# Optimization experiments

Measured on AMD Instinct MI355X. Metric: run time of the kernel, lower is better.

The kernel has to match this reference:

```python
import jax, jax.numpy as jnp
import numpy as np

B, T, I = 256, 512, 1024
H, O = 1024, 1024


def setup_inputs() -> dict:
    key = jax.random.key(0)
    ks = jax.random.split(key, 8)
    std = 1.0 / np.sqrt(H)
    u = lambda k, shape: jax.random.uniform(k, shape, jnp.float32, -std, std)
    return {
        "x": jax.random.normal(ks[0], (B, T, I), jnp.float32),
        "Wx": u(ks[1], (4 * H, I)),   # x2h weight
        "bx": u(ks[2], (4 * H,)),     # x2h bias
        "Wh": u(ks[3], (4 * H, H)),   # h2h weight
        "bh": u(ks[4], (4 * H,)),     # h2h bias
        "c2c": u(ks[5], (3 * H,)),    # peephole weights (ci, cf, co)
        "Wfc": u(ks[6], (O, H)),      # final fc weight
        "bfc": u(ks[7], (O,)),        # final fc bias
    }


def reference(x, Wx, bx, Wh, bh, c2c, Wfc, bfc):
    Bv, Tv, _ = x.shape
    Hv = Wh.shape[1]
    # Precompute input projections for all timesteps in one GEMM: [B, T, 4H]
    xg = jnp.einsum('bti,gi->btg', x, Wx) + bx + bh
    ci, cf, co = jnp.split(c2c, 3)

    def step(carry, xg_t):
        h, c = carry                      # [B, H] each
        gates = xg_t + h @ Wh.T           # [B, 4H]
        i, f, g, o = jnp.split(gates, 4, axis=-1)
        i = jax.nn.sigmoid(i + ci * c)    # peephole into input gate
        f = jax.nn.sigmoid(f + cf * c)    # peephole into forget gate
        c_new = f * c + i * jnp.tanh(g)
        o = jax.nn.sigmoid(o + co * c_new)  # peephole into output gate
        h_new = o * jnp.tanh(c_new)
        return (h_new, c_new), None

    h0 = jnp.zeros((Bv, Hv), x.dtype)
    c0 = jnp.zeros((Bv, Hv), x.dtype)
    (hT, _), _ = jax.lax.scan(step, (h0, c0), jnp.swapaxes(xg, 0, 1))
    return hT @ Wfc.T + bfc  # [B, O]
```

## Files before the change

kernel.cpp:

```cpp
#include <hip/hip_runtime.h>
#include <hip/hip_bf16.h>

typedef __attribute__((ext_vector_type(8))) short short8;
typedef __attribute__((ext_vector_type(4))) float f32x4;

#define T_STEPS 512
#define BATCH   256
#define HDIM    1024
#define GDIM    4096

__device__ __forceinline__ float sigmoidf_(float x) {
  return 1.0f / (1.0f + __expf(-x));
}
__device__ __forceinline__ float tanh_(float x) {
  return 2.0f / (1.0f + __expf(-2.0f * x)) - 1.0f;
}
__device__ __forceinline__ short f2bf(float f) {
  __hip_bfloat16 h = __float2bfloat16(f);
  short s;
  __builtin_memcpy(&s, &h, sizeof(short));
  return s;
}

__global__ void pack_kernel(const float* __restrict__ Wh,
                            const float* __restrict__ bx, const float* __restrict__ bh,
                            __hip_bfloat16* __restrict__ Whb,
                            float* __restrict__ biasc)
{
  const int stride = gridDim.x * blockDim.x;
  const int tid0 = blockIdx.x * blockDim.x + threadIdx.x;
  for (int i = tid0; i < GDIM * HDIM; i += stride)
    Whb[i] = __float2bfloat16(Wh[i]);
  for (int i = tid0; i < GDIM; i += stride)
    biasc[i] = bx[i] + bh[i];
}

__global__ __launch_bounds__(512, 1)
void xg_gemm(const float* __restrict__ x, const float* __restrict__ Wx,
             __hip_bfloat16* __restrict__ xg, int t0)
{
  __shared__ short8 As[2][1024];
  __shared__ short8 Bs[2][1024];

  const int tid  = threadIdx.x;
  const int wave = tid >> 6;
  const int lane = tid & 63;

  const int cpx = gridDim.x >> 3;
  const int nb  = (blockIdx.x & 7) * cpx + (blockIdx.x >> 3);
  const int nt  = nb & 31;
  const int mt  = nb >> 5;

  const int trel  = mt >> 1;
  const int brow0 = (mt & 1) * 128;

  const int r0 = tid >> 3;
  const int cg = tid & 7;

  const float* asrc0 = x + ((size_t)(brow0 + r0) * T_STEPS + (t0 + trel)) * 1024 + cg * 8;
  const float* asrc1 = x + ((size_t)(brow0 + r0 + 64) * T_STEPS + (t0 + trel)) * 1024 + cg * 8;
  const float* bsrc0 = Wx + (size_t)(nt * 128 + r0) * 1024 + cg * 8;
  const float* bsrc1 = Wx + (size_t)(nt * 128 + r0 + 64) * 1024 + cg * 8;

  const int aslot0 = r0 * 8 + (cg ^ (r0 & 7));
  const int aslot1 = (r0 + 64) * 8 + (cg ^ (r0 & 7));

  f32x4 a0l, a0h, a1l, a1h, b0l, b0h, b1l, b1h;

#define XG_LOAD(KC)                                        \
  do {                                                     \
    a0l = *(const f32x4*)(asrc0 + (KC) * 64);              \
    a0h = *(const f32x4*)(asrc0 + (KC) * 64 + 4);          \
    a1l = *(const f32x4*)(asrc1 + (KC) * 64);              \
    a1h = *(const f32x4*)(asrc1 + (KC) * 64 + 4);          \
    b0l = *(const f32x4*)(bsrc0 + (KC) * 64);              \
    b0h = *(const f32x4*)(bsrc0 + (KC) * 64 + 4);          \
    b1l = *(const f32x4*)(bsrc1 + (KC) * 64);              \
    b1h = *(const f32x4*)(bsrc1 + (KC) * 64 + 4);          \
  } while (0)

#define XG_CVT1(lo, hi, dstarr, slot)                      \
  do {                                                     \
    short8 s_;                                             \
    _Pragma("unroll")                                      \
    for (int e = 0; e < 4; ++e) {                          \
      s_[e]     = f2bf((lo)[e]);                           \
      s_[e + 4] = f2bf((hi)[e]);                           \
    }                                                      \
    dstarr[slot] = s_;                                     \
  } while (0)

#define XG_WRITE(BUF)                                      \
  do {                                                     \
    XG_CVT1(a0l, a0h, As[BUF], aslot0);                    \
    XG_CVT1(a1l, a1h, As[BUF], aslot1);                    \
    XG_CVT1(b0l, b0h, Bs[BUF], aslot0);                    \
    XG_CVT1(b1l, b1h, Bs[BUF], aslot1);                    \
  } while (0)

  const int wr = wave >> 2;
  const int wc = wave & 3;

  f32x4 acc[4][2];
#pragma unroll
  for (int m = 0; m < 4; ++m)
#pragma unroll
    for (int n = 0; n < 2; ++n) acc[m][n] = (f32x4){0.f, 0.f, 0.f, 0.f};

  XG_LOAD(0);
  XG_WRITE(0);
  __syncthreads();

#pragma unroll 1
  for (int kc = 0; kc < 16; ++kc) {
    if (kc < 15) XG_LOAD(kc + 1);
    const int bs = kc & 1;
#pragma unroll
    for (int ks = 0; ks < 2; ++ks) {
      const int cgf = ks * 4 + (lane >> 4);
      short8 af[4], bfr[2];
#pragma unroll
      for (int m = 0; m < 4; ++m) {
        const int row = wr * 64 + m * 16 + (lane & 15);
        af[m] = As[bs][row * 8 + (cgf ^ (row & 7))];
      }
#pragma unroll
      for (int n = 0; n < 2; ++n) {
        const int row = wc * 32 + n * 16 + (lane & 15);
        bfr[n] = Bs[bs][row * 8 + (cgf ^ (row & 7))];
      }
#pragma unroll
      for (int m = 0; m < 4; ++m)
#pragma unroll
        for (int n = 0; n < 2; ++n)
          acc[m][n] = __builtin_amdgcn_mfma_f32_16x16x32_bf16(af[m], bfr[n], acc[m][n], 0, 0, 0);
    }
    if (kc < 15) XG_WRITE((kc + 1) & 1);
    __syncthreads();
  }

  const int dcol = lane & 15;
  const int dr0  = (lane >> 4) * 4;
#pragma unroll
  for (int m = 0; m < 4; ++m) {
#pragma unroll
    for (int n = 0; n < 2; ++n) {
      const int ocol = nt * 128 + wc * 32 + n * 16 + dcol;
#pragma unroll
      for (int rr = 0; rr < 4; ++rr) {
        const int orow = mt * 128 + wr * 64 + m * 16 + dr0 + rr;
        xg[(size_t)orow * GDIM + ocol] = __float2bfloat16(acc[m][n][rr]);
      }
    }
  }
#undef XG_LOAD
#undef XG_CVT1
#undef XG_WRITE
}

__global__ __launch_bounds__(512, 1)
void lstm_step(const __hip_bfloat16* __restrict__ xg_t,
               const __hip_bfloat16* __restrict__ Whb,
               const float* __restrict__ biasc,
               const float* __restrict__ c2c,
               const __hip_bfloat16* __restrict__ h_in,
               __hip_bfloat16* __restrict__ h_out,
               float* __restrict__ c_st)
{
  __shared__ short8 As[2][1024];
  __shared__ short8 Bs[2][1024];

  const int tid  = threadIdx.x;
  const int wave = tid >> 6;
  const int lane = tid & 63;

  const int bid   = blockIdx.x;
  const int xcd   = bid & 7;
  const int idx   = bid >> 3;
  const int ntile = xcd * 8 + (idx & 7);
  const int mtile = idx >> 3;
  const int b0 = mtile * 64;
  const int j0 = ntile * 16;

  const int r0  = tid >> 4;
  const int cg0 = tid & 15;

  const int aslot0 = r0 * 16 + (cg0 ^ (r0 & 7));
  const int aslot1 = (r0 + 32) * 16 + (cg0 ^ (r0 & 7));

  const int Brow0 = ((r0 >> 4)     ) * HDIM + j0 + (r0 & 15);
  const int Brow1 = ((r0 >> 4) + 2 ) * HDIM + j0 + (r0 & 15);
  const __hip_bfloat16* Wp0 = Whb + (size_t)Brow0 * HDIM + cg0 * 8;
  const __hip_bfloat16* Wp1 = Whb + (size_t)Brow1 * HDIM + cg0 * 8;
  const __hip_bfloat16* hp0 = h_in + (size_t)(b0 + r0) * HDIM + cg0 * 8;
  const __hip_bfloat16* hp1 = h_in + (size_t)(b0 + r0 + 32) * HDIM + cg0 * 8;

  short8 hv0, hv1, bv0, bv1;

#define LOADS(KC)                                                   \
  do {                                                              \
    bv0 = *(const short8*)(const void*)(Wp0 + (size_t)(KC) * 128);  \
    bv1 = *(const short8*)(const void*)(Wp1 + (size_t)(KC) * 128);  \
    hv0 = *(const short8*)(const void*)(hp0 + (size_t)(KC) * 128);  \
    hv1 = *(const short8*)(const void*)(hp1 + (size_t)(KC) * 128);  \
  } while (0)

#define WRITE_LDS(BUF)                                              \
  do {                                                              \
    As[BUF][aslot0] = hv0;                                          \
    As[BUF][aslot1] = hv1;                                          \
    Bs[BUF][aslot0] = bv0;                                          \
    Bs[BUF][aslot1] = bv1;                                          \
  } while (0)

  const int rf = wave & 3;
  const int kh = wave >> 2;
  const int arow = rf * 16 + (lane & 15);

  f32x4 acc[4];
#pragma unroll
  for (int f = 0; f < 4; ++f) acc[f] = (f32x4){0.f, 0.f, 0.f, 0.f};

  LOADS(0);
  WRITE_LDS(0);
  __syncthreads();

#pragma unroll 1
  for (int kc = 0; kc < 8; ++kc) {
    if (kc < 7) LOADS(kc + 1);
    const int bs = kc & 1;
#pragma unroll
    for (int ss = 0; ss < 2; ++ss) {
      const int colg = kh * 8 + ss * 4 + (lane >> 4);
      short8 af = As[bs][arow * 16 + (colg ^ (arow & 7))];
#pragma unroll
      for (int f = 0; f < 4; ++f) {
        const int br = f * 16 + (lane & 15);
        short8 bfq = Bs[bs][br * 16 + (colg ^ (br & 7))];
        acc[f] = __builtin_amdgcn_mfma_f32_16x16x32_bf16(af, bfq, acc[f], 0, 0, 0);
      }
    }
    if (kc < 7) WRITE_LDS((kc + 1) & 1);
    __syncthreads();
  }

  float* red = (float*)&As[0][0];
  const int drow = (lane >> 4) * 4;
  const int dcol = lane & 15;
  if (kh == 1) {
#pragma unroll
    for (int f = 0; f < 4; ++f)
#pragma unroll
      for (int r = 0; r < 4; ++r)
        red[(rf * 16 + drow + r) * 64 + f * 16 + dcol] = acc[f][r];
  }
  __syncthreads();
  if (kh == 0) {
#pragma unroll
    for (int f = 0; f < 4; ++f)
#pragma unroll
      for (int r = 0; r < 4; ++r)
        acc[f][r] += red[(rf * 16 + drow + r) * 64 + f * 16 + dcol];

    const int j = j0 + dcol;
    const float bi = biasc[j];
    const float bf = biasc[HDIM + j];
    const float bg = biasc[2 * HDIM + j];
    const float bo = biasc[3 * HDIM + j];
    const float ci = c2c[j];
    const float cf = c2c[HDIM + j];
    const float co = c2c[2 * HDIM + j];
#pragma unroll
    for (int r = 0; r < 4; ++r) {
      const int b = b0 + rf * 16 + drow + r;
      const __hip_bfloat16* xr = xg_t + (size_t)b * GDIM + j;
      float x0 = __bfloat162float(xr[0]);
      float x1 = __bfloat162float(xr[HDIM]);
      float x2 = __bfloat162float(xr[2 * HDIM]);
      float x3 = __bfloat162float(xr[3 * HDIM]);
      float cp = c_st[(size_t)b * HDIM + j];
      float ig = sigmoidf_(acc[0][r] + x0 + bi + ci * cp);
      float fg = sigmoidf_(acc[1][r] + x1 + bf + cf * cp);
      float gg = tanh_(acc[2][r] + x2 + bg);
      float cn = fg * cp + ig * gg;
      float og = sigmoidf_(acc[3][r] + x3 + bo + co * cn);
      float hn = og * tanh_(cn);
      c_st[(size_t)b * HDIM + j] = cn;
      h_out[(size_t)b * HDIM + j] = __float2bfloat16(hn);
    }
  }
#undef LOADS
#undef WRITE_LDS
}

__global__ __launch_bounds__(256, 1)
void fc_kernel(const __hip_bfloat16* __restrict__ h,
               const float* __restrict__ Wfc,
               const float* __restrict__ bfc,
               float* __restrict__ out)
{
  __shared__ short8 As8[512];
  __shared__ short8 Bs8[512];

  const int tid = threadIdx.x;
  const int wave = tid >> 6;
  const int lane = tid & 63;
  const int mtile = blockIdx.x >> 4;
  const int otile = blockIdx.x & 15;
  const int b0 = mtile * 64, o0 = otile * 64;

  const int r0 = tid >> 3;
  const int cg0 = tid & 7;

  f32x4 acc[4];
#pragma unroll
  for (int f = 0; f < 4; ++f) acc[f] = (f32x4){0.f, 0.f, 0.f, 0.f};

#pragma unroll 1
  for (int kc = 0; kc < 16; ++kc) {
    __syncthreads();
    As8[r0 * 8 + (cg0 ^ (r0 & 7))] =
        *(const short8*)(const void*)(h + (size_t)(b0 + r0) * HDIM + kc * 64 + cg0 * 8);
    As8[(r0 + 32) * 8 + (cg0 ^ (r0 & 7))] =
        *(const short8*)(const void*)(h + (size_t)(b0 + r0 + 32) * HDIM + kc * 64 + cg0 * 8);
    {
      const float* p0 = Wfc + (size_t)(o0 + r0) * HDIM + kc * 64 + cg0 * 8;
      const float* p1 = Wfc + (size_t)(o0 + r0 + 32) * HDIM + kc * 64 + cg0 * 8;
      f32x4 l0 = *(const f32x4*)p0, h0 = *(const f32x4*)(p0 + 4);
      f32x4 l1 = *(const f32x4*)p1, h1 = *(const f32x4*)(p1 + 4);
      short8 s0, s1;
#pragma unroll
      for (int e = 0; e < 4; ++e) {
        s0[e] = f2bf(l0[e]); s0[e + 4] = f2bf(h0[e]);
        s1[e] = f2bf(l1[e]); s1[e + 4] = f2bf(h1[e]);
      }
      Bs8[r0 * 8 + (cg0 ^ (r0 & 7))] = s0;
      Bs8[(r0 + 32) * 8 + (cg0 ^ (r0 & 7))] = s1;
    }
    __syncthreads();
#pragma unroll
    for (int s = 0; s < 2; ++s) {
      const int colg = s * 4 + (lane >> 4);
      const int ar = wave * 16 + (lane & 15);
      short8 af = As8[ar * 8 + (colg ^ (ar & 7))];
#pragma unroll
      for (int f = 0; f < 4; ++f) {
        const int br = f * 16 + (lane & 15);
        short8 bfq = Bs8[br * 8 + (colg ^ (br & 7))];
        acc[f] = __builtin_amdgcn_mfma_f32_16x16x32_bf16(af, bfq, acc[f], 0, 0, 0);
      }
    }
  }

  const int dcol = lane & 15;
  const int drow = (lane >> 4) * 4;
#pragma unroll
  for (int f = 0; f < 4; ++f) {
    const int o = o0 + f * 16 + dcol;
    const float bias = bfc[o];
#pragma unroll
    for (int r = 0; r < 4; ++r) {
      const int b = b0 + wave * 16 + drow + r;
      out[(size_t)b * 1024 + o] = acc[f][r] + bias;
    }
  }
}

extern "C" void kernel_launch(void* const* d_in, const int* in_sizes, int n_in,
                              void* d_out, int out_size, void* d_ws, size_t ws_size,
                              hipStream_t stream)
{
  const float* x   = (const float*)d_in[0];
  const float* Wx  = (const float*)d_in[1];
  const float* bx  = (const float*)d_in[2];
  const float* Wh  = (const float*)d_in[3];
  const float* bh  = (const float*)d_in[4];
  const float* c2c = (const float*)d_in[5];
  const float* Wfc = (const float*)d_in[6];
  const float* bfc = (const float*)d_in[7];
  float* out = (float*)d_out;

  char* ws = (char*)d_ws;
  __hip_bfloat16* Whb   = (__hip_bfloat16*)(ws);
  float*          biasc = (float*)(ws + (8u << 20));
  __hip_bfloat16* hb0   = (__hip_bfloat16*)(ws + (8u << 20) + (1u << 16));
  __hip_bfloat16* hb1   = (__hip_bfloat16*)(ws + (8u << 20) + (1u << 16) + (1u << 19));
  float*          c_st  = (float*)(ws + (8u << 20) + (1u << 16) + (1u << 20));
  __hip_bfloat16* xgbuf = (__hip_bfloat16*)(ws + (11u << 20));

  const size_t xg_off = (size_t)11 << 20;
  int W = 4;
  for (int cand = 512; cand >= 4; cand >>= 1) {
    size_t need = xg_off + (size_t)cand * BATCH * GDIM * sizeof(__hip_bfloat16);
    if (need <= ws_size) { W = cand; break; }
  }

  hipMemsetAsync(hb0, 0, (size_t)BATCH * HDIM * sizeof(__hip_bfloat16), stream);
  hipMemsetAsync(c_st, 0, (size_t)BATCH * HDIM * sizeof(float), stream);

  pack_kernel<<<1024, 256, 0, stream>>>(Wh, bx, bh, Whb, biasc);

  const int NW = T_STEPS / W;
  for (int w = 0; w < NW; ++w) {
    xg_gemm<<<W * 64, 512, 0, stream>>>(x, Wx, xgbuf, w * W);
    for (int tt = 0; tt < W; ++tt) {
      const int t = w * W + tt;
      const __hip_bfloat16* hin = (t & 1) ? hb1 : hb0;
      __hip_bfloat16* hout      = (t & 1) ? hb0 : hb1;
      lstm_step<<<256, 512, 0, stream>>>(xgbuf + (size_t)tt * BATCH * GDIM,
                                         Whb, biasc, c2c, hin, hout, c_st);
    }
  }

  fc_kernel<<<64, 256, 0, stream>>>(hb0, Wfc, bfc, out);
}
```

Measured before the change: 8.063 ms.

## Make LSTM recurrence persistent with grid barriers and LDS-resident Wh slices

Replaces the per-timestep lstm_step launches with a persistent kernel that loops over a window of timesteps. Each block keeps its Wh slice resident in LDS, keeps the cell state in registers, and synchronizes with a custom per-XCD hierarchical atomic grid barrier. Wx is also pre-converted to bf16 once in pack_kernel, so xg_gemm loads half the weight bytes and skips per-tile conversion. This removes launch overhead and repeated Wh global reloads every step. In exchange it relies on all 256 blocks being co-resident to avoid deadlock, and the LDS footprint grows to about 144KB.

```diff
diff --git a/kernel.cpp b/kernel.cpp
--- a/kernel.cpp
+++ b/kernel.cpp
@@ -22,21 +22,52 @@
   return s;
 }
 
-__global__ void pack_kernel(const float* __restrict__ Wh,
+__device__ __forceinline__ void grid_barrier(unsigned* bar, int grp) {
+  __syncthreads();
+  if (threadIdx.x == 0) {
+    __threadfence();
+    unsigned* gcnt = bar + (size_t)grp * 32;
+    unsigned* gctr = bar + 8 * 32;
+    unsigned* gen  = bar + 8 * 32 + 32;
+    unsigned g = __hip_atomic_load(gen, __ATOMIC_RELAXED, __HIP_MEMORY_SCOPE_AGENT);
+    unsigned a = __hip_atomic_fetch_add(gcnt, 1u, __ATOMIC_ACQ_REL, __HIP_MEMORY_SCOPE_AGENT);
+    if (a == 31u) {
+      __hip_atomic_store(gcnt, 0u, __ATOMIC_RELAXED, __HIP_MEMORY_SCOPE_AGENT);
+      unsigned ga = __hip_atomic_fetch_add(gctr, 1u, __ATOMIC_ACQ_REL, __HIP_MEMORY_SCOPE_AGENT);
+      if (ga == 7u) {
+        __hip_atomic_store(gctr, 0u, __ATOMIC_RELAXED, __HIP_MEMORY_SCOPE_AGENT);
+        __hip_atomic_store(gen, g + 1u, __ATOMIC_RELEASE, __HIP_MEMORY_SCOPE_AGENT);
+      } else {
+        while (__hip_atomic_load(gen, __ATOMIC_RELAXED, __HIP_MEMORY_SCOPE_AGENT) == g)
+          __builtin_amdgcn_s_sleep(1);
+      }
+    } else {
+      while (__hip_atomic_load(gen, __ATOMIC_RELAXED, __HIP_MEMORY_SCOPE_AGENT) == g)
+        __builtin_amdgcn_s_sleep(1);
+    }
+    __threadfence();
+  }
+  __syncthreads();
+}
+
+__global__ void pack_kernel(const float* __restrict__ Wh, const float* __restrict__ Wx,
                             const float* __restrict__ bx, const float* __restrict__ bh,
                             __hip_bfloat16* __restrict__ Whb,
+                            __hip_bfloat16* __restrict__ Wxb,
                             float* __restrict__ biasc)
 {
   const int stride = gridDim.x * blockDim.x;
   const int tid0 = blockIdx.x * blockDim.x + threadIdx.x;
-  for (int i = tid0; i < GDIM * HDIM; i += stride)
+  for (int i = tid0; i < GDIM * HDIM; i += stride) {
     Whb[i] = __float2bfloat16(Wh[i]);
+    Wxb[i] = __float2bfloat16(Wx[i]);
+  }
   for (int i = tid0; i < GDIM; i += stride)
     biasc[i] = bx[i] + bh[i];
 }
 
 __global__ __launch_bounds__(512, 1)
-void xg_gemm(const float* __restrict__ x, const float* __restrict__ Wx,
+void xg_gemm(const float* __restrict__ x, const __hip_bfloat16* __restrict__ Wxb,
              __hip_bfloat16* __restrict__ xg, int t0)
 {
   __shared__ short8 As[2][1024];
@@ -59,13 +90,14 @@
 
   const float* asrc0 = x + ((size_t)(brow0 + r0) * T_STEPS + (t0 + trel)) * 1024 + cg * 8;
   const float* asrc1 = x + ((size_t)(brow0 + r0 + 64) * T_STEPS + (t0 + trel)) * 1024 + cg * 8;
-  const float* bsrc0 = Wx + (size_t)(nt * 128 + r0) * 1024 + cg * 8;
-  const float* bsrc1 = Wx + (size_t)(nt * 128 + r0 + 64) * 1024 + cg * 8;
+  const __hip_bfloat16* bsrc0 = Wxb + (size_t)(nt * 128 + r0) * 1024 + cg * 8;
+  const __hip_bfloat16* bsrc1 = Wxb + (size_t)(nt * 128 + r0 + 64) * 1024 + cg * 8;
 
   const int aslot0 = r0 * 8 + (cg ^ (r0 & 7));
   const int aslot1 = (r0 + 64) * 8 + (cg ^ (r0 & 7));
 
-  f32x4 a0l, a0h, a1l, a1h, b0l, b0h, b1l, b1h;
+  f32x4 a0l, a0h, a1l, a1h;
+  short8 bv0, bv1;
 
 #define XG_LOAD(KC)                                        \
   do {                                                     \
@@ -73,29 +105,22 @@
     a0h = *(const f32x4*)(asrc0 + (KC) * 64 + 4);          \
     a1l = *(const f32x4*)(asrc1 + (KC) * 64);              \
     a1h = *(const f32x4*)(asrc1 + (KC) * 64 + 4);          \
-    b0l = *(const f32x4*)(bsrc0 + (KC) * 64);              \
-    b0h = *(const f32x4*)(bsrc0 + (KC) * 64 + 4);          \
-    b1l = *(const f32x4*)(bsrc1 + (KC) * 64);              \
-    b1h = *(const f32x4*)(bsrc1 + (KC) * 64 + 4);          \
+    bv0 = *(const short8*)(const void*)(bsrc0 + (KC) * 64);\
+    bv1 = *(const short8*)(const void*)(bsrc1 + (KC) * 64);\
   } while (0)
 
-#define XG_CVT1(lo, hi, dstarr, slot)                      \
+#define XG_WRITE(BUF)                                      \
   do {                                                     \
-    short8 s_;                                             \
+    short8 s0_, s1_;                                       \
     _Pragma("unroll")                                      \
     for (int e = 0; e < 4; ++e) {                          \
-      s_[e]     = f2bf((lo)[e]);                           \
-      s_[e + 4] = f2bf((hi)[e]);                           \
+      s0_[e] = f2bf(a0l[e]); s0_[e + 4] = f2bf(a0h[e]);    \
+      s1_[e] = f2bf(a1l[e]); s1_[e + 4] = f2bf(a1h[e]);    \
     }                                                      \
-    dstarr[slot] = s_;                                     \
-  } while (0)
-
-#define XG_WRITE(BUF)                                      \
-  do {                                                     \
-    XG_CVT1(a0l, a0h, As[BUF], aslot0);                    \
-    XG_CVT1(a1l, a1h, As[BUF], aslot1);                    \
-    XG_CVT1(b0l, b0h, Bs[BUF], aslot0);                    \
-    XG_CVT1(b1l, b1h, Bs[BUF], aslot1);                    \
+    As[BUF][aslot0] = s0_;                                 \
+    As[BUF][aslot1] = s1_;                                 \
+    Bs[BUF][aslot0] = bv0;                                 \
+    Bs[BUF][aslot1] = bv1;                                 \
   } while (0)
 
   const int wr = wave >> 2;
@@ -154,21 +179,22 @@
     }
   }
 #undef XG_LOAD
-#undef XG_CVT1
 #undef XG_WRITE
 }
 
 __global__ __launch_bounds__(512, 1)
-void lstm_step(const __hip_bfloat16* __restrict__ xg_t,
-               const __hip_bfloat16* __restrict__ Whb,
-               const float* __restrict__ biasc,
-               const float* __restrict__ c2c,
-               const __hip_bfloat16* __restrict__ h_in,
-               __hip_bfloat16* __restrict__ h_out,
-               float* __restrict__ c_st)
+void lstm_persist(const __hip_bfloat16* __restrict__ xg,
+                  const __hip_bfloat16* __restrict__ Whb,
+                  const float* __restrict__ biasc,
+                  const float* __restrict__ c2c,
+                  __hip_bfloat16* __restrict__ hb0,
+                  __hip_bfloat16* __restrict__ hb1,
+                  float* __restrict__ c_st,
+                  unsigned* __restrict__ bar,
+                  int W)
 {
-  __shared__ short8 As[2][1024];
-  __shared__ short8 Bs[2][1024];
+  __shared__ short8 Bp[8192];
+  __shared__ short8 As[2][512];
 
   const int tid  = threadIdx.x;
   const int wave = tid >> 6;
@@ -182,115 +208,121 @@
   const int b0 = mtile * 64;
   const int j0 = ntile * 16;
 
-  const int r0  = tid >> 4;
-  const int cg0 = tid & 15;
-
-  const int aslot0 = r0 * 16 + (cg0 ^ (r0 & 7));
-  const int aslot1 = (r0 + 32) * 16 + (cg0 ^ (r0 & 7));
-
-  const int Brow0 = ((r0 >> 4)     ) * HDIM + j0 + (r0 & 15);
-  const int Brow1 = ((r0 >> 4) + 2 ) * HDIM + j0 + (r0 & 15);
-  const __hip_bfloat16* Wp0 = Whb + (size_t)Brow0 * HDIM + cg0 * 8;
-  const __hip_bfloat16* Wp1 = Whb + (size_t)Brow1 * HDIM + cg0 * 8;
-  const __hip_bfloat16* hp0 = h_in + (size_t)(b0 + r0) * HDIM + cg0 * 8;
-  const __hip_bfloat16* hp1 = h_in + (size_t)(b0 + r0 + 32) * HDIM + cg0 * 8;
-
-  short8 hv0, hv1, bv0, bv1;
-
-#define LOADS(KC)                                                   \
-  do {                                                              \
-    bv0 = *(const short8*)(const void*)(Wp0 + (size_t)(KC) * 128);  \
-    bv1 = *(const short8*)(const void*)(Wp1 + (size_t)(KC) * 128);  \
-    hv0 = *(const short8*)(const void*)(hp0 + (size_t)(KC) * 128);  \
-    hv1 = *(const short8*)(const void*)(hp1 + (size_t)(KC) * 128);  \
-  } while (0)
-
-#define WRITE_LDS(BUF)                                              \
-  do {                                                              \
-    As[BUF][aslot0] = hv0;                                          \
-    As[BUF][aslot1] = hv1;                                          \
-    Bs[BUF][aslot0] = bv0;                                          \
-    Bs[BUF][aslot1] = bv1;                                          \
-  } while (0)
+  for (int i = tid; i < 8192; i += 512) {
+    const int row = i >> 7, ck = i & 127;
+    const int grow = (row >> 4) * HDIM + j0 + (row & 15);
+    Bp[row * 128 + (ck ^ (row & 7))] =
+        *(const short8*)(const void*)(Whb + (size_t)grow * HDIM + ck * 8);
+  }
+
+  const int r0  = tid >> 3;
+  const int cg0 = tid & 7;
+  const int aslot = r0 * 8 + (cg0 ^ (r0 & 7));
+  const size_t hoff = (size_t)(b0 + r0) * HDIM + cg0 * 8;
 
   const int rf = wave & 3;
   const int kh = wave >> 2;
   const int arow = rf * 16 + (lane & 15);
-
-  f32x4 acc[4];
-#pragma unroll
-  for (int f = 0; f < 4; ++f) acc[f] = (f32x4){0.f, 0.f, 0.f, 0.f};
-
-  LOADS(0);
-  WRITE_LDS(0);
+  const int colg = kh * 4 + (lane >> 4);
+  const int aridx = arow * 8 + (colg ^ (arow & 7));
+  int bbase[4];
+#pragma unroll
+  for (int f = 0; f < 4; ++f) {
+    const int br = f * 16 + (lane & 15);
+    bbase[f] = br * 128 + (colg ^ (br & 7));
+  }
+
+  const int dcol = lane & 15;
+  const int drow = (lane >> 4) * 4;
+  const int jj = j0 + dcol;
+  const float bi  = biasc[jj];
+  const float bfv = biasc[HDIM + jj];
+  const float bg  = biasc[2 * HDIM + jj];
+  const float bo  = biasc[3 * HDIM + jj];
+  const float ci  = c2c[jj];
+  const float cf  = c2c[HDIM + jj];
+  const float co  = c2c[2 * HDIM + jj];
+  const int eb0 = b0 + rf * 16 + drow;
+
+  float c_reg[4];
+#pragma unroll
+  for (int r = 0; r < 4; ++r)
+    c_reg[r] = c_st[(size_t)(eb0 + r) * HDIM + jj];
+
   __syncthreads();
 
 #pragma unroll 1
-  for (int kc = 0; kc < 8; ++kc) {
-    if (kc < 7) LOADS(kc + 1);
-    const int bs = kc & 1;
-#pragma unroll
-    for (int ss = 0; ss < 2; ++ss) {
-      const int colg = kh * 8 + ss * 4 + (lane >> 4);
-      short8 af = As[bs][arow * 16 + (colg ^ (arow & 7))];
-#pragma unroll
-      for (int f = 0; f < 4; ++f) {
-        const int br = f * 16 + (lane & 15);
-        short8 bfq = Bs[bs][br * 16 + (colg ^ (br & 7))];
-        acc[f] = __builtin_amdgcn_mfma_f32_16x16x32_bf16(af, bfq, acc[f], 0, 0, 0);
-      }
-    }
-    if (kc < 7) WRITE_LDS((kc + 1) & 1);
+  for (int s = 0; s < W; ++s) {
+    const __hip_bfloat16* hin = (s & 1) ? hb1 : hb0;
+    __hip_bfloat16* hout      = (s & 1) ? hb0 : hb1;
+
+    short8 hv[16];
+    const __hip_bfloat16* hp = hin + hoff;
+#pragma unroll
+    for (int kc = 0; kc < 16; ++kc)
+      hv[kc] = *(const short8*)(const void*)(hp + kc * 64);
+
+    const __hip_bfloat16* xr = xg + (size_t)s * BATCH * GDIM;
+    float xgv[4][4];
+    if (kh == 0) {
+#pragma unroll
+      for (int r = 0; r < 4; ++r)
+#pragma unroll
+        for (int f = 0; f < 4; ++f)
+          xgv[r][f] = __bfloat162float(xr[(size_t)(eb0 + r) * GDIM + f * HDIM + jj]);
+    }
+
+    f32x4 acc[4];
+#pragma unroll
+    for (int f = 0; f < 4; ++f) acc[f] = (f32x4){0.f, 0.f, 0.f, 0.f};
+
+    As[0][aslot] = hv[0];
     __syncthreads();
-  }
-
-  float* red = (float*)&As[0][0];
-  const int drow = (lane >> 4) * 4;
-  const int dcol = lane & 15;
-  if (kh == 1) {
-#pragma unroll
-    for (int f = 0; f < 4; ++f)
-#pragma unroll
-      for (int r = 0; r < 4; ++r)
-        red[(rf * 16 + drow + r) * 64 + f * 16 + dcol] = acc[f][r];
-  }
-  __syncthreads();
+#pragma unroll
+    for (int kc = 0; kc < 16; ++kc) {
+      short8 af = As[kc & 1][aridx];
+#pragma unroll
+      for (int f = 0; f < 4; ++f)
+        acc[f] = __builtin_amdgcn_mfma_f32_16x16x32_bf16(af, Bp[bbase[f] + kc * 8], acc[f], 0, 0, 0);
+      if (kc < 15) As[(kc + 1) & 1][aslot] = hv[kc + 1];
+      __syncthreads();
+    }
+
+    float* red = (float*)&As[0][0];
+    if (kh == 1) {
+#pragma unroll
+      for (int f = 0; f < 4; ++f)
+#pragma unroll
+        for (int r = 0; r < 4; ++r)
+          red[(rf * 16 + drow + r) * 64 + f * 16 + dcol] = acc[f][r];
+    }
+    __syncthreads();
+    if (kh == 0) {
+#pragma unroll
+      for (int r = 0; r < 4; ++r) {
+        const int rr = (rf * 16 + drow + r) * 64 + dcol;
+        float gI = acc[0][r] + red[rr +  0] + xgv[r][0] + bi;
+        float gF = acc[1][r] + red[rr + 16] + xgv[r][1] + bfv;
+        float gG = acc[2][r] + red[rr + 32] + xgv[r][2] + bg;
+        float gO = acc[3][r] + red[rr + 48] + xgv[r][3] + bo;
+        float cp = c_reg[r];
+        float ig = sigmoidf_(gI + ci * cp);
+        float fg = sigmoidf_(gF + cf * cp);
+        float gg = tanh_(gG);
+        float cn = fg * cp + ig * gg;
+        float og = sigmoidf_(gO + co * cn);
+        c_reg[r] = cn;
+        hout[(size_t)(eb0 + r) * HDIM + jj] = __float2bfloat16(og * tanh_(cn));
+      }
+    }
+    if (s < W - 1) grid_barrier(bar, xcd);
+  }
+
   if (kh == 0) {
 #pragma unroll
-    for (int f = 0; f < 4; ++f)
-#pragma unroll
-      for (int r = 0; r < 4; ++r)
-        acc[f][r] += red[(rf * 16 + drow + r) * 64 + f * 16 + dcol];
-
-    const int j = j0 + dcol;
-    const float bi = biasc[j];
-    const float bf = biasc[HDIM + j];
-    const float bg = biasc[2 * HDIM + j];
-    const float bo = biasc[3 * HDIM + j];
-    const float ci = c2c[j];
-    const float cf = c2c[HDIM + j];
-    const float co = c2c[2 * HDIM + j];
-#pragma unroll
-    for (int r = 0; r < 4; ++r) {
-      const int b = b0 + rf * 16 + drow + r;
-      const __hip_bfloat16* xr = xg_t + (size_t)b * GDIM + j;
-      float x0 = __bfloat162float(xr[0]);
-      float x1 = __bfloat162float(xr[HDIM]);
-      float x2 = __bfloat162float(xr[2 * HDIM]);
-      float x3 = __bfloat162float(xr[3 * HDIM]);
-      float cp = c_st[(size_t)b * HDIM + j];
-      float ig = sigmoidf_(acc[0][r] + x0 + bi + ci * cp);
-      float fg = sigmoidf_(acc[1][r] + x1 + bf + cf * cp);
-      float gg = tanh_(acc[2][r] + x2 + bg);
-      float cn = fg * cp + ig * gg;
-      float og = sigmoidf_(acc[3][r] + x3 + bo + co * cn);
-      float hn = og * tanh_(cn);
-      c_st[(size_t)b * HDIM + j] = cn;
-      h_out[(size_t)b * HDIM + j] = __float2bfloat16(hn);
-    }
-  }
-#undef LOADS
-#undef WRITE_LDS
+    for (int r = 0; r < 4; ++r)
+      c_st[(size_t)(eb0 + r) * HDIM + jj] = c_reg[r];
+  }
 }
 
 __global__ __launch_bounds__(256, 1)
@@ -382,34 +414,31 @@
 
   char* ws = (char*)d_ws;
   __hip_bfloat16* Whb   = (__hip_bfloat16*)(ws);
-  float*          biasc = (float*)(ws + (8u << 20));
-  __hip_bfloat16* hb0   = (__hip_bfloat16*)(ws + (8u << 20) + (1u << 16));
-  __hip_bfloat16* hb1   = (__hip_bfloat16*)(ws + (8u << 20) + (1u << 16) + (1u << 19));
-  float*          c_st  = (float*)(ws + (8u << 20) + (1u << 16) + (1u << 20));
-  __hip_bfloat16* xgbuf = (__hip_bfloat16*)(ws + (11u << 20));
-
-  const size_t xg_off = (size_t)11 << 20;
-  int W = 4;
-  for (int cand = 512; cand >= 4; cand >>= 1) {
+  __hip_bfloat16* Wxb   = (__hip_bfloat16*)(ws + (8u << 20));
+  float*          biasc = (float*)(ws + (16u << 20));
+  __hip_bfloat16* hb0   = (__hip_bfloat16*)(ws + (16u << 20) + (1u << 16));
+  __hip_bfloat16* hb1   = (__hip_bfloat16*)(ws + (16u << 20) + (1u << 16) + (1u << 19));
+  float*          c_st  = (float*)(ws + (17u << 20) + (1u << 16));
+  unsigned*       bar   = (unsigned*)(ws + (18u << 20) + (1u << 16));
+  __hip_bfloat16* xgbuf = (__hip_bfloat16*)(ws + (19u << 20));
+
+  const size_t xg_off = (size_t)19 << 20;
+  int W = 2;
+  for (int cand = 512; cand >= 2; cand >>= 1) {
     size_t need = xg_off + (size_t)cand * BATCH * GDIM * sizeof(__hip_bfloat16);
     if (need <= ws_size) { W = cand; break; }
   }
 
   hipMemsetAsync(hb0, 0, (size_t)BATCH * HDIM * sizeof(__hip_bfloat16), stream);
   hipMemsetAsync(c_st, 0, (size_t)BATCH * HDIM * sizeof(float), stream);
-
-  pack_kernel<<<1024, 256, 0, stream>>>(Wh, bx, bh, Whb, biasc);
+  hipMemsetAsync(bar, 0, 4096, stream);
+
+  pack_kernel<<<1024, 256, 0, stream>>>(Wh, Wx, bx, bh, Whb, Wxb, biasc);
 
   const int NW = T_STEPS / W;
   for (int w = 0; w < NW; ++w) {
-    xg_gemm<<<W * 64, 512, 0, stream>>>(x, Wx, xgbuf, w * W);
-    for (int tt = 0; tt < W; ++tt) {
-      const int t = w * W + tt;
-      const __hip_bfloat16* hin = (t & 1) ? hb1 : hb0;
-      __hip_bfloat16* hout      = (t & 1) ? hb0 : hb1;
-      lstm_step<<<256, 512, 0, stream>>>(xgbuf + (size_t)tt * BATCH * GDIM,
-                                         Whb, biasc, c2c, hin, hout, c_st);
-    }
+    xg_gemm<<<W * 64, 512, 0, stream>>>(x, Wxb, xgbuf, w * W);
+    lstm_persist<<<256, 512, 0, stream>>>(xgbuf, Whb, biasc, c2c, hb0, hb1, c_st, bar, W);
   }
 
   fc_kernel<<<64, 256, 0, stream>>>(hb0, Wfc, bfc, out);
```

After: 14.89 ms. 1.85x slower.

## Load LSTM step tiles directly into LDS with smaller double-buffered K chunks

Applied to the files above, without the earlier changes.

The recurrent step kernel now uses global_load_lds to stream h and Wh tiles straight into shared memory, with the XOR swizzle applied on the global source address. Previously the data was staged through registers. The K chunk is halved to 64, so there are 16 fully unrolled iterations with one MFMA row per wave and half the LDS footprint. Launch bounds are also raised for both the step kernel and the xg GEMM. This is meant to cut register staging and load latency on each timestep, at the cost of twice as many barriers per step.

```diff
diff --git a/kernel.cpp b/kernel.cpp
--- a/kernel.cpp
+++ b/kernel.cpp
@@ -20,6 +20,12 @@
   short s;
   __builtin_memcpy(&s, &h, sizeof(short));
   return s;
+}
+
+__device__ __forceinline__ void gld_lds16(const __hip_bfloat16* g, void* l) {
+  __builtin_amdgcn_global_load_lds(
+      (const __attribute__((address_space(1))) void*)(const void*)g,
+      (__attribute__((address_space(3))) void*)l, 16, 0, 0);
 }
 
 __global__ void pack_kernel(const float* __restrict__ Wh,
@@ -35,7 +41,7 @@
     biasc[i] = bx[i] + bh[i];
 }
 
-__global__ __launch_bounds__(512, 1)
+__global__ __launch_bounds__(512, 2)
 void xg_gemm(const float* __restrict__ x, const float* __restrict__ Wx,
              __hip_bfloat16* __restrict__ xg, int t0)
 {
@@ -158,7 +164,7 @@
 #undef XG_WRITE
 }
 
-__global__ __launch_bounds__(512, 1)
+__global__ __launch_bounds__(512, 4)
 void lstm_step(const __hip_bfloat16* __restrict__ xg_t,
                const __hip_bfloat16* __restrict__ Whb,
                const float* __restrict__ biasc,
@@ -167,12 +173,14 @@
                __hip_bfloat16* __restrict__ h_out,
                float* __restrict__ c_st)
 {
-  __shared__ short8 As[2][1024];
-  __shared__ short8 Bs[2][1024];
+  __shared__ short8 As[2][512];
+  __shared__ short8 Bs[2][512];
 
   const int tid  = threadIdx.x;
   const int wave = tid >> 6;
   const int lane = tid & 63;
+  const int l15  = lane & 15;
+  const int lg   = lane >> 4;
 
   const int bid   = blockIdx.x;
   const int xcd   = bid & 7;
@@ -182,71 +190,57 @@
   const int b0 = mtile * 64;
   const int j0 = ntile * 16;
 
-  const int r0  = tid >> 4;
-  const int cg0 = tid & 15;
-
-  const int aslot0 = r0 * 16 + (cg0 ^ (r0 & 7));
-  const int aslot1 = (r0 + 32) * 16 + (cg0 ^ (r0 & 7));
-
-  const int Brow0 = ((r0 >> 4)     ) * HDIM + j0 + (r0 & 15);
-  const int Brow1 = ((r0 >> 4) + 2 ) * HDIM + j0 + (r0 & 15);
-  const __hip_bfloat16* Wp0 = Whb + (size_t)Brow0 * HDIM + cg0 * 8;
-  const __hip_bfloat16* Wp1 = Whb + (size_t)Brow1 * HDIM + cg0 * 8;
-  const __hip_bfloat16* hp0 = h_in + (size_t)(b0 + r0) * HDIM + cg0 * 8;
-  const __hip_bfloat16* hp1 = h_in + (size_t)(b0 + r0 + 32) * HDIM + cg0 * 8;
-
-  short8 hv0, hv1, bv0, bv1;
-
-#define LOADS(KC)                                                   \
-  do {                                                              \
-    bv0 = *(const short8*)(const void*)(Wp0 + (size_t)(KC) * 128);  \
-    bv1 = *(const short8*)(const void*)(Wp1 + (size_t)(KC) * 128);  \
-    hv0 = *(const short8*)(const void*)(hp0 + (size_t)(KC) * 128);  \
-    hv1 = *(const short8*)(const void*)(hp1 + (size_t)(KC) * 128);  \
-  } while (0)
-
-#define WRITE_LDS(BUF)                                              \
-  do {                                                              \
-    As[BUF][aslot0] = hv0;                                          \
-    As[BUF][aslot1] = hv1;                                          \
-    Bs[BUF][aslot0] = bv0;                                          \
-    Bs[BUF][aslot1] = bv1;                                          \
-  } while (0)
+  const int srow = tid >> 3;
+  const int scg  = tid & 7;
+  const int sswz = scg ^ (srow & 7);
+  const __hip_bfloat16* asrc = h_in + (size_t)(b0 + srow) * HDIM + sswz * 8;
+  const int bgrow = (srow >> 4) * HDIM + j0 + (srow & 15);
+  const __hip_bfloat16* bsrc = Whb + (size_t)bgrow * HDIM + sswz * 8;
+
+  void* la0 = (void*)&As[0][wave * 64];
+  void* la1 = (void*)&As[1][wave * 64];
+  void* lb0 = (void*)&Bs[0][wave * 64];
+  void* lb1 = (void*)&Bs[1][wave * 64];
 
   const int rf = wave & 3;
   const int kh = wave >> 2;
-  const int arow = rf * 16 + (lane & 15);
+  const int arow = rf * 16 + l15;
+  const int colg = kh * 4 + lg;
+  const int aidx = arow * 8 + (colg ^ (arow & 7));
+  int bidx[4];
+#pragma unroll
+  for (int f = 0; f < 4; ++f) {
+    const int br = f * 16 + l15;
+    bidx[f] = br * 8 + (colg ^ (br & 7));
+  }
 
   f32x4 acc[4];
 #pragma unroll
   for (int f = 0; f < 4; ++f) acc[f] = (f32x4){0.f, 0.f, 0.f, 0.f};
 
-  LOADS(0);
-  WRITE_LDS(0);
+  gld_lds16(asrc, la0);
+  gld_lds16(bsrc, lb0);
   __syncthreads();
 
-#pragma unroll 1
-  for (int kc = 0; kc < 8; ++kc) {
-    if (kc < 7) LOADS(kc + 1);
-    const int bs = kc & 1;
-#pragma unroll
-    for (int ss = 0; ss < 2; ++ss) {
-      const int colg = kh * 8 + ss * 4 + (lane >> 4);
-      short8 af = As[bs][arow * 16 + (colg ^ (arow & 7))];
-#pragma unroll
-      for (int f = 0; f < 4; ++f) {
-        const int br = f * 16 + (lane & 15);
-        short8 bfq = Bs[bs][br * 16 + (colg ^ (br & 7))];
-        acc[f] = __builtin_amdgcn_mfma_f32_16x16x32_bf16(af, bfq, acc[f], 0, 0, 0);
-      }
-    }
-    if (kc < 7) WRITE_LDS((kc + 1) & 1);
+#pragma unroll
+  for (int kc = 0; kc < 16; ++kc) {
+    if (kc < 15) {
+      gld_lds16(asrc + (kc + 1) * 64, (kc & 1) ? la0 : la1);
+      gld_lds16(bsrc + (kc + 1) * 64, (kc & 1) ? lb0 : lb1);
+    }
+    const short8* Ab = As[kc & 1];
+    const short8* Bb = Bs[kc & 1];
+    short8 af = Ab[aidx];
+    acc[0] = __builtin_amdgcn_mfma_f32_16x16x32_bf16(af, Bb[bidx[0]], acc[0], 0, 0, 0);
+    acc[1] = __builtin_amdgcn_mfma_f32_16x16x32_bf16(af, Bb[bidx[1]], acc[1], 0, 0, 0);
+    acc[2] = __builtin_amdgcn_mfma_f32_16x16x32_bf16(af, Bb[bidx[2]], acc[2], 0, 0, 0);
+    acc[3] = __builtin_amdgcn_mfma_f32_16x16x32_bf16(af, Bb[bidx[3]], acc[3], 0, 0, 0);
     __syncthreads();
   }
 
   float* red = (float*)&As[0][0];
-  const int drow = (lane >> 4) * 4;
-  const int dcol = lane & 15;
+  const int drow = lg * 4;
+  const int dcol = l15;
   if (kh == 1) {
 #pragma unroll
     for (int f = 0; f < 4; ++f)
@@ -289,8 +283,6 @@
       h_out[(size_t)b * HDIM + j] = __float2bfloat16(hn);
     }
   }
-#undef LOADS
-#undef WRITE_LDS
 }
 
 __global__ __launch_bounds__(256, 1)
```

Result: slower. 9.412 ms (+16.7%).
